# Kernel tuning notes

Measured on AMD Instinct MI355X. Metric: run time of the kernel, lower is better.

## Reference

```python
import jax, jax.numpy as jnp
import numpy as np

B, S, H = 4, 2048, 1024
NH = 16
HD = H // NH  # 64
EPS = 1e-12


def setup_inputs() -> dict:
    key = jax.random.key(0)
    ks = jax.random.split(key, 10)
    sc = 1.0 / np.sqrt(H)
    return {
        "hidden_states": jax.random.normal(ks[0], (B, S, H), jnp.float32),
        "attention_mask": jnp.ones((B, S), jnp.float32),
        "Wq": jax.random.normal(ks[1], (H, H), jnp.float32) * sc,
        "bq": jnp.zeros((H,), jnp.float32),
        "Wk": jax.random.normal(ks[2], (H, H), jnp.float32) * sc,
        "bk": jnp.zeros((H,), jnp.float32),
        "Wv": jax.random.normal(ks[3], (H, H), jnp.float32) * sc,
        "bv": jnp.zeros((H,), jnp.float32),
        "Wd": jax.random.normal(ks[4], (H, H), jnp.float32) * sc,
        "bd": jnp.zeros((H,), jnp.float32),
        "ln_g": jnp.ones((H,), jnp.float32),
        "ln_b": jnp.zeros((H,), jnp.float32),
    }


def reference(hidden_states, attention_mask, Wq, bq, Wk, bk, Wv, bv, Wd, bd, ln_g, ln_b):
    def heads(x):  # [B,S,H] -> [B,NH,S,HD]
        return x.reshape(B, S, NH, HD).transpose(0, 2, 1, 3)

    q = heads(hidden_states @ Wq.T + bq)
    k = heads(hidden_states @ Wk.T + bk)
    v = heads(hidden_states @ Wv.T + bv)

    scores = jnp.einsum('bhqd,bhkd->bhqk', q, k) / np.sqrt(HD).astype(np.float32)
    # 2D mask -> [B,1,1,S]; (1-m)*-10000 additive bias
    bias = (1.0 - attention_mask)[:, None, None, :] * -10000.0
    probs = jax.nn.softmax(scores + bias, axis=-1)  # dropout p=0 -> identity

    ctx = jnp.einsum('bhqk,bhkd->bhqd', probs, v)
    ctx = ctx.transpose(0, 2, 1, 3).reshape(B, S, H)

    out = ctx @ Wd.T + bd
    x = out + hidden_states
    mu = jnp.mean(x, axis=-1, keepdims=True)
    var = jnp.mean(jnp.square(x - mu), axis=-1, keepdims=True)
    return (x - mu) * jax.lax.rsqrt(var + EPS) * ln_g + ln_b
```

## Files before the change

kernel.cpp:

```cpp
#include <hip/hip_runtime.h>
#include <stdint.h>

#define B_ 4
#define S_ 2048
#define H_ 1024
#define NH_ 16
#define HD_ 64

typedef __bf16 bf16x8 __attribute__((ext_vector_type(8)));
typedef unsigned short u16x8 __attribute__((ext_vector_type(8)));
typedef float f32x4 __attribute__((ext_vector_type(4)));
typedef float f32x16 __attribute__((ext_vector_type(16)));

__device__ __forceinline__ unsigned short f2bf(float x) {
  union { float f; unsigned u; } c; c.f = x;
  unsigned r = (c.u + 0x7FFFu + ((c.u >> 16) & 1u)) >> 16;
  return (unsigned short)r;
}

__device__ __forceinline__ unsigned cvtpk(float lo, float hi) {
  unsigned r;
  asm("v_cvt_pk_bf16_f32 %0, %1, %2" : "=v"(r) : "v"(lo), "v"(hi));
  return r;
}

__device__ __forceinline__ void gload16(const unsigned short* g, unsigned short* lds) {
  __builtin_amdgcn_global_load_lds((const __attribute__((address_space(1))) void*)g,
                                   (__attribute__((address_space(3))) void*)lds, 16, 0, 0);
}

__global__ __launch_bounds__(256) void cvt_kernel(const float* __restrict__ src,
                                                  unsigned short* __restrict__ dst, int n) {
  int i = (blockIdx.x * blockDim.x + threadIdx.x) * 4;
  if (i < n) {
    float4 v = *reinterpret_cast<const float4*>(src + i);
    ushort4 o;
    o.x = f2bf(v.x); o.y = f2bf(v.y); o.z = f2bf(v.z); o.w = f2bf(v.w);
    *reinterpret_cast<ushort4*>(dst + i) = o;
  }
}

__global__ __launch_bounds__(256) void cvtw_kernel(const float* __restrict__ w0,
                                                   const float* __restrict__ w1,
                                                   const float* __restrict__ w2,
                                                   const float* __restrict__ w3,
                                                   unsigned short* __restrict__ o0,
                                                   unsigned short* __restrict__ o1,
                                                   unsigned short* __restrict__ o2,
                                                   unsigned short* __restrict__ o3, int n) {
  const int which = blockIdx.y;
  const float* src = (which == 0) ? w0 : (which == 1) ? w1 : (which == 2) ? w2 : w3;
  unsigned short* dst = (which == 0) ? o0 : (which == 1) ? o1 : (which == 2) ? o2 : o3;
  int i = (blockIdx.x * blockDim.x + threadIdx.x) * 4;
  if (i < n) {
    float4 v = *reinterpret_cast<const float4*>(src + i);
    ushort4 o;
    o.x = f2bf(v.x); o.y = f2bf(v.y); o.z = f2bf(v.z); o.w = f2bf(v.w);
    *reinterpret_cast<ushort4*>(dst + i) = o;
  }
}

template <bool BF16OUT>
__global__ __launch_bounds__(256) void gemm_bt(const unsigned short* __restrict__ A,
                                               const unsigned short* __restrict__ Bm,
                                               const float* __restrict__ bias,
                                               void* __restrict__ Cout,
                                               int M, int N, int K) {
  __shared__ unsigned short As[128 * 32];
  __shared__ unsigned short Bs[128 * 32];
  const int t = threadIdx.x;
  const int lane = t & 63;
  const int wv = t >> 6;
  const int wm = wv >> 1, wn = wv & 1;
  const int m0 = blockIdx.x * 128, n0 = blockIdx.y * 128;
  const int l15 = lane & 15, g8 = (lane >> 4) * 8;

  f32x4 acc[4][4];
#pragma unroll
  for (int i = 0; i < 4; ++i)
#pragma unroll
    for (int j = 0; j < 4; ++j) { f32x4 z = {0.f, 0.f, 0.f, 0.f}; acc[i][j] = z; }

  const int rowA = t >> 2;
  const int colA = (t & 3) * 8;
  const unsigned short* gA0 = A + (long)(m0 + rowA) * K + colA;
  const unsigned short* gA1 = A + (long)(m0 + 64 + rowA) * K + colA;
  const unsigned short* gB0 = Bm + (long)(n0 + rowA) * K + colA;
  const unsigned short* gB1 = Bm + (long)(n0 + 64 + rowA) * K + colA;
  unsigned short* ldsA0 = &As[wv * 512];
  unsigned short* ldsA1 = &As[2048 + wv * 512];
  unsigned short* ldsB0 = &Bs[wv * 512];
  unsigned short* ldsB1 = &Bs[2048 + wv * 512];

  for (int k0 = 0; k0 < K; k0 += 32) {
    __syncthreads();
    gload16(gA0 + k0, ldsA0);
    gload16(gA1 + k0, ldsA1);
    gload16(gB0 + k0, ldsB0);
    gload16(gB1 + k0, ldsB1);
    __syncthreads();

    bf16x8 af[4], bfr[4];
#pragma unroll
    for (int i = 0; i < 4; ++i)
      af[i] = *reinterpret_cast<const bf16x8*>(&As[(wm * 64 + i * 16 + l15) * 32 + g8]);
#pragma unroll
    for (int j = 0; j < 4; ++j)
      bfr[j] = *reinterpret_cast<const bf16x8*>(&Bs[(wn * 64 + j * 16 + l15) * 32 + g8]);
#pragma unroll
    for (int i = 0; i < 4; ++i)
#pragma unroll
      for (int j = 0; j < 4; ++j)
        acc[i][j] = __builtin_amdgcn_mfma_f32_16x16x32_bf16(af[i], bfr[j], acc[i][j], 0, 0, 0);
  }

  const int r0 = (lane >> 4) * 4;
#pragma unroll
  for (int i = 0; i < 4; ++i)
#pragma unroll
    for (int j = 0; j < 4; ++j) {
      int col = n0 + wn * 64 + j * 16 + l15;
      float bv = bias[col];
#pragma unroll
      for (int r = 0; r < 4; ++r) {
        int row = m0 + wm * 64 + i * 16 + r0 + r;
        float v = acc[i][j][r] + bv;
        if (BF16OUT)
          ((unsigned short*)Cout)[(long)row * N + col] = f2bf(v);
        else
          ((float*)Cout)[(long)row * N + col] = v;
      }
    }
}

__global__ __launch_bounds__(256) void attn_kernel(const unsigned short* __restrict__ Q,
                                                   const unsigned short* __restrict__ Kg,
                                                   const unsigned short* __restrict__ Vg,
                                                   const float* __restrict__ mask,
                                                   unsigned short* __restrict__ ctx) {
  __shared__ __align__(16) unsigned short Kt[2][64 * 64];
  __shared__ __align__(16) unsigned short VtT[2][64 * 72];
  __shared__ __align__(16) float biasL[2][64];
  __shared__ __align__(16) float alBuf[4][32];
  __shared__ int mflag[2];
  __shared__ int anyMsh;

  const int t = threadIdx.x, lane = t & 63;
  const int wv = t >> 6;
  const int id = blockIdx.x;
  const int bh = ((id >> 7) << 3) | (id & 7);
  const int qb = (id >> 3) & 15;
  const int h = bh & 15, b = bh >> 4;
  const int q0w = qb * 128 + wv * 32;
  const int l31 = lane & 31, h2 = lane >> 5;
  const long headoff = (long)h * HD_;
  const float L2E = 1.44269504088896f;
  const float SC = 0.125f * L2E;

  if (t == 0) anyMsh = 0;
  __syncthreads();
  {
    bool nz = false;
    for (int i = t; i < S_; i += 256) nz |= (mask[(long)b * S_ + i] != 1.0f);
    if (__any(nz) && lane == 0) atomicOr(&anyMsh, 1);
  }

  bf16x8 qf[4];
  {
    const unsigned short* Qrow = Q + ((long)(b * S_ + q0w + l31)) * H_ + headoff;
#pragma unroll
    for (int c = 0; c < 4; ++c) {
      bf16x8 raw = *reinterpret_cast<const bf16x8*>(Qrow + 16 * c + 8 * h2);
#pragma unroll
      for (int j = 0; j < 8; ++j) qf[c][j] = (__bf16)((float)raw[j] * SC);
    }
  }
  __syncthreads();
  const bool anyM = (anyMsh != 0);

  f32x16 o[2];
#pragma unroll
  for (int dt = 0; dt < 2; ++dt)
#pragma unroll
    for (int r = 0; r < 16; ++r) o[dt][r] = 0.f;
  float mrow = -1.0e30f, lsum = 0.f;

  int koff[4];
#pragma unroll
  for (int c = 0; c < 4; ++c) koff[c] = 8 * ((2 * c + h2) ^ (l31 & 7));

  const int rowd0 = l31, rowd1 = 32 + l31;
  const int grp0 = (rowd0 >> 3) & 7, grp1 = (rowd1 >> 3) & 7;
  int voff0[4], voff1[4];
#pragma unroll
  for (int kc = 0; kc < 4; ++kc) {
    voff0[kc] = rowd0 * 72 + 8 * ((2 * kc + h2) ^ grp0);
    voff1[kc] = rowd1 * 72 + 8 * ((2 * kc + h2) ^ grp1);
  }

  const long gbase = (long)(b * S_) * H_ + headoff;

  const unsigned short* kg0 =
      Kg + gbase + (long)(16 * wv + (lane >> 3)) * H_ + 8 * ((lane & 7) ^ (lane >> 3));
  const unsigned short* kg1 = kg0 + 8 * H_;

  const int vrow = (t >> 3) * 2, dc = t & 7;
  u16x8 vr0, vr1;

  auto LOADK = [&](int buf, int kv0) {
    gload16(kg0 + (long)kv0 * H_, &Kt[buf][(16 * wv) * 64]);
    gload16(kg1 + (long)kv0 * H_, &Kt[buf][(16 * wv + 8) * 64]);
  };
  auto LOADV = [&](int kv0) {
    vr0 = *reinterpret_cast<const u16x8*>(Vg + gbase + (long)(kv0 + vrow) * H_ + dc * 8);
    vr1 = *reinterpret_cast<const u16x8*>(Vg + gbase + (long)(kv0 + vrow + 1) * H_ + dc * 8);
  };
  auto WRITEV = [&](int buf, int kv0) {
    const int pos = (vrow & 7) | (((vrow >> 3) ^ dc) << 3);
#pragma unroll
    for (int j = 0; j < 8; ++j) {
      ushort2 pr; pr.x = vr0[j]; pr.y = vr1[j];
      *reinterpret_cast<ushort2*>(&VtT[buf][(dc * 8 + j) * 72 + pos]) = pr;
    }
    if (anyM && t < 64) {
      float mv = mask[(long)b * S_ + kv0 + t];
      biasL[buf][t] = (1.f - mv) * (-10000.f * L2E);
      unsigned long long bal = __ballot(mv != 1.0f);
      if (t == 0) mflag[buf] = (bal != 0ull);
    }
  };

  auto SMPV = [&](f32x16& sv, int kvt, int cur) {
    float m0 = fmaxf(fmaxf(sv[0], sv[1]), sv[2]);
    float m1 = fmaxf(fmaxf(sv[3], sv[4]), sv[5]);
    float m2 = fmaxf(fmaxf(sv[6], sv[7]), sv[8]);
    float m3 = fmaxf(fmaxf(sv[9], sv[10]), sv[11]);
    float m4 = fmaxf(fmaxf(sv[12], sv[13]), sv[14]);
    float t0 = fmaxf(fmaxf(m0, m1), m2);
    float t1 = fmaxf(fmaxf(m3, m4), sv[15]);
    float tm = fmaxf(t0, t1);
    tm = fmaxf(tm, __shfl_xor(tm, 32));
    if (!__all(tm <= mrow + 8.0f)) {
      float mn = fmaxf(mrow, tm);
      float al = exp2f(mrow - mn);
      mrow = mn;
      lsum *= al;
      if (lane < 32) alBuf[wv][lane] = al;
      __builtin_amdgcn_wave_barrier();
#pragma unroll
      for (int m = 0; m < 4; ++m) {
        f32x4 av = *reinterpret_cast<const f32x4*>(&alBuf[wv][8 * m + 4 * h2]);
#pragma unroll
        for (int i = 0; i < 4; ++i) {
          o[0][4 * m + i] *= av[i];
          o[1][4 * m + i] *= av[i];
        }
      }
    }
#pragma unroll
    for (int r = 0; r < 16; ++r) sv[r] = exp2f(sv[r] - mrow);
    {
      float s0 = sv[0] + sv[1], s1 = sv[2] + sv[3], s2 = sv[4] + sv[5], s3 = sv[6] + sv[7];
      float s4 = sv[8] + sv[9], s5 = sv[10] + sv[11], s6 = sv[12] + sv[13], s7 = sv[14] + sv[15];
      float u0 = s0 + s1, u1 = s2 + s3, u2 = s4 + s5, u3 = s6 + s7;
      float ts = (u0 + u1) + (u2 + u3);
      ts += __shfl_xor(ts, 32);
      lsum += ts;
    }
#pragma unroll
    for (int c2 = 0; c2 < 2; ++c2) {
      const int kc = 2 * kvt + c2;
      unsigned p0 = cvtpk(sv[8 * c2 + 0], sv[8 * c2 + 1]);
      unsigned p1 = cvtpk(sv[8 * c2 + 2], sv[8 * c2 + 3]);
      unsigned p2 = cvtpk(sv[8 * c2 + 4], sv[8 * c2 + 5]);
      unsigned p3 = cvtpk(sv[8 * c2 + 6], sv[8 * c2 + 7]);
      asm("v_permlane32_swap_b32 %0, %1" : "+v"(p0), "+v"(p2));
      asm("v_permlane32_swap_b32 %0, %1" : "+v"(p1), "+v"(p3));
      union { unsigned w[4]; bf16x8 v; } fa;
      fa.w[0] = p0; fa.w[1] = p1; fa.w[2] = p2; fa.w[3] = p3;

      bf16x8 vb0 = *reinterpret_cast<const bf16x8*>(&VtT[cur][voff0[kc]]);
      bf16x8 vb1 = *reinterpret_cast<const bf16x8*>(&VtT[cur][voff1[kc]]);
      __builtin_amdgcn_s_setprio(1);
      o[0] = __builtin_amdgcn_mfma_f32_32x32x16_bf16(fa.v, vb0, o[0], 0, 0, 0);
      o[1] = __builtin_amdgcn_mfma_f32_32x32x16_bf16(fa.v, vb1, o[1], 0, 0, 0);
      __builtin_amdgcn_s_setprio(0);
    }
  };

  const int NT = S_ / 64;
  LOADK(0, 0);
  LOADV(0);
  WRITEV(0, 0);
  __syncthreads();

  for (int it = 0; it < NT; ++it) {
    const int cur = it & 1;
    const bool more = (it + 1 < NT);
    if (more) {
      LOADK(cur ^ 1, (it + 1) * 64);
      LOADV((it + 1) * 64);
    }

#pragma unroll
    for (int kvt = 0; kvt < 2; ++kvt) {
      f32x16 sv;
#pragma unroll
      for (int r = 0; r < 16; ++r) sv[r] = 0.f;
      const int rb = (kvt * 32 + l31) * 64;
      __builtin_amdgcn_s_setprio(1);
#pragma unroll
      for (int c = 0; c < 4; ++c) {
        bf16x8 af = *reinterpret_cast<const bf16x8*>(&Kt[cur][rb + koff[c]]);
        sv = __builtin_amdgcn_mfma_f32_32x32x16_bf16(af, qf[c], sv, 0, 0, 0);
      }
      __builtin_amdgcn_s_setprio(0);
      if (anyM && mflag[cur]) {
#pragma unroll
        for (int m = 0; m < 4; ++m) {
          f32x4 bb = *reinterpret_cast<const f32x4*>(&biasL[cur][kvt * 32 + 8 * m + 4 * h2]);
#pragma unroll
          for (int i = 0; i < 4; ++i) sv[4 * m + i] += bb[i];
        }
      }
      SMPV(sv, kvt, cur);
    }

    if (more) {
      WRITEV(cur ^ 1, (it + 1) * 64);
      __syncthreads();
    }
  }

  if (lane < 32) alBuf[wv][lane] = 1.0f / lsum;
  __builtin_amdgcn_wave_barrier();
  unsigned short* ctxbase = ctx + ((long)(b * S_ + q0w + 4 * h2)) * H_ + headoff + l31;
#pragma unroll
  for (int m = 0; m < 4; ++m) {
    f32x4 iv = *reinterpret_cast<const f32x4*>(&alBuf[wv][8 * m + 4 * h2]);
#pragma unroll
    for (int i = 0; i < 4; ++i) {
#pragma unroll
      for (int dt = 0; dt < 2; ++dt)
        ctxbase[(long)(8 * m + i) * H_ + dt * 32] = f2bf(o[dt][4 * m + i] * iv[i]);
    }
  }
}

__global__ __launch_bounds__(256) void ln_kernel(const float* __restrict__ proj,
                                                 const float* __restrict__ hs,
                                                 const float* __restrict__ gam,
                                                 const float* __restrict__ bet,
                                                 float* __restrict__ out) {
  const int row = blockIdx.x;
  const int t = threadIdx.x;
  const long base = (long)row * H_ + t * 4;
  float4 a = *reinterpret_cast<const float4*>(proj + base);
  float4 hv = *reinterpret_cast<const float4*>(hs + base);
  float x0 = a.x + hv.x, x1 = a.y + hv.y, x2 = a.z + hv.z, x3 = a.w + hv.w;
  float s1 = x0 + x1 + x2 + x3;
  float s2 = x0 * x0 + x1 * x1 + x2 * x2 + x3 * x3;
#pragma unroll
  for (int off = 1; off < 64; off <<= 1) {
    s1 += __shfl_xor(s1, off);
    s2 += __shfl_xor(s2, off);
  }
  __shared__ float a1[4], a2[4];
  if ((t & 63) == 0) { a1[t >> 6] = s1; a2[t >> 6] = s2; }
  __syncthreads();
  float ts1 = a1[0] + a1[1] + a1[2] + a1[3];
  float ts2 = a2[0] + a2[1] + a2[2] + a2[3];
  float mu = ts1 * (1.0f / H_);
  float var = ts2 * (1.0f / H_) - mu * mu;
  float inv = rsqrtf(var + 1e-12f);
  float4 gv = *reinterpret_cast<const float4*>(gam + t * 4);
  float4 bb = *reinterpret_cast<const float4*>(bet + t * 4);
  float4 ov;
  ov.x = (x0 - mu) * inv * gv.x + bb.x;
  ov.y = (x1 - mu) * inv * gv.y + bb.y;
  ov.z = (x2 - mu) * inv * gv.z + bb.z;
  ov.w = (x3 - mu) * inv * gv.w + bb.w;
  *reinterpret_cast<float4*>(out + base) = ov;
}

extern "C" void kernel_launch(void* const* d_in, const int* in_sizes, int n_in,
                              void* d_out, int out_size, void* d_ws, size_t ws_size,
                              hipStream_t stream) {
  const float* hs   = (const float*)d_in[0];
  const float* mask = (const float*)d_in[1];
  const float* Wq   = (const float*)d_in[2];
  const float* bq   = (const float*)d_in[3];
  const float* Wk   = (const float*)d_in[4];
  const float* bk   = (const float*)d_in[5];
  const float* Wv   = (const float*)d_in[6];
  const float* bv   = (const float*)d_in[7];
  const float* Wd   = (const float*)d_in[8];
  const float* bd   = (const float*)d_in[9];
  const float* lng  = (const float*)d_in[10];
  const float* lnb  = (const float*)d_in[11];
  float* out = (float*)d_out;

  char* ws = (char*)d_ws;
  const size_t SZ_X = (size_t)B_ * S_ * H_ * 2;
  const size_t SZ_W = (size_t)H_ * H_ * 2;
  unsigned short* Xb  = (unsigned short*)(ws);
  unsigned short* Wqb = (unsigned short*)(ws + SZ_X);
  unsigned short* Wkb = (unsigned short*)(ws + SZ_X + SZ_W);
  unsigned short* Wvb = (unsigned short*)(ws + SZ_X + 2 * SZ_W);
  unsigned short* Wdb = (unsigned short*)(ws + SZ_X + 3 * SZ_W);
  unsigned short* Qb  = (unsigned short*)(ws + SZ_X + 4 * SZ_W);
  unsigned short* Kb  = (unsigned short*)(ws + 2 * SZ_X + 4 * SZ_W);
  unsigned short* Vb  = (unsigned short*)(ws + 3 * SZ_X + 4 * SZ_W);
  unsigned short* Cxb = (unsigned short*)(ws + 4 * SZ_X + 4 * SZ_W);
  float* Proj         = (float*)(ws + 5 * SZ_X + 4 * SZ_W);

  const int NX = B_ * S_ * H_;
  const int NW = H_ * H_;

  cvt_kernel<<<NX / 1024, 256, 0, stream>>>(hs, Xb, NX);
  dim3 gw(NW / 1024, 4);
  cvtw_kernel<<<gw, 256, 0, stream>>>(Wq, Wk, Wv, Wd, Wqb, Wkb, Wvb, Wdb, NW);

  dim3 gg(B_ * S_ / 128, H_ / 128);
  gemm_bt<true><<<gg, 256, 0, stream>>>(Xb, Wqb, bq, Qb, B_ * S_, H_, H_);
  gemm_bt<true><<<gg, 256, 0, stream>>>(Xb, Wkb, bk, Kb, B_ * S_, H_, H_);
  gemm_bt<true><<<gg, 256, 0, stream>>>(Xb, Wvb, bv, Vb, B_ * S_, H_, H_);

  attn_kernel<<<dim3((S_ / 128) * NH_ * B_), 256, 0, stream>>>(Qb, Kb, Vb, mask, Cxb);

  gemm_bt<false><<<gg, 256, 0, stream>>>(Cxb, Wdb, bd, Proj, B_ * S_, H_, H_);

  ln_kernel<<<B_ * S_, 256, 0, stream>>>(Proj, hs, lng, lnb, out);
}
```

Measured before the change: 292.8 us.

## Fuse QKV projections into one GEMM and restructure attention score loop

Concatenates the Q, K and V weights and biases into a single 3072-wide matrix so one GEMM launch produces an interleaved QKV buffer, which the attention kernel reads with a 3072 row stride. This removes two kernel launches and gives the GEMM a larger grid for better occupancy. The attention loop now issues both 32-row score MFMA groups before running softmax, and the cross-half reductions use v_permlane32_swap instead of shuffles. The cost is strided K/V/Q reads from the wider rows and higher register pressure from holding two score tiles at once.

```diff
diff --git a/kernel.cpp b/kernel.cpp
--- a/kernel.cpp
+++ b/kernel.cpp
@@ -6,6 +6,7 @@
 #define H_ 1024
 #define NH_ 16
 #define HD_ 64
+#define KS_ 3072
 
 typedef __bf16 bf16x8 __attribute__((ext_vector_type(8)));
 typedef unsigned short u16x8 __attribute__((ext_vector_type(8)));
@@ -22,6 +23,17 @@
   unsigned r;
   asm("v_cvt_pk_bf16_f32 %0, %1, %2" : "=v"(r) : "v"(lo), "v"(hi));
   return r;
+}
+
+__device__ __forceinline__ float xmax32(float x) {
+  float a = x, b = x;
+  asm("v_permlane32_swap_b32 %0, %1" : "+v"(a), "+v"(b));
+  return fmaxf(a, b);
+}
+__device__ __forceinline__ float xadd32(float x) {
+  float a = x, b = x;
+  asm("v_permlane32_swap_b32 %0, %1" : "+v"(a), "+v"(b));
+  return a + b;
 }
 
 __device__ __forceinline__ void gload16(const unsigned short* g, unsigned short* lds) {
@@ -44,19 +56,25 @@
                                                    const float* __restrict__ w1,
                                                    const float* __restrict__ w2,
                                                    const float* __restrict__ w3,
-                                                   unsigned short* __restrict__ o0,
-                                                   unsigned short* __restrict__ o1,
-                                                   unsigned short* __restrict__ o2,
-                                                   unsigned short* __restrict__ o3, int n) {
+                                                   const float* __restrict__ bq,
+                                                   const float* __restrict__ bk,
+                                                   const float* __restrict__ bv,
+                                                   unsigned short* __restrict__ wqkv,
+                                                   unsigned short* __restrict__ wd,
+                                                   float* __restrict__ bcat, int n) {
   const int which = blockIdx.y;
   const float* src = (which == 0) ? w0 : (which == 1) ? w1 : (which == 2) ? w2 : w3;
-  unsigned short* dst = (which == 0) ? o0 : (which == 1) ? o1 : (which == 2) ? o2 : o3;
+  unsigned short* dst = (which < 3) ? (wqkv + (size_t)which * n) : wd;
   int i = (blockIdx.x * blockDim.x + threadIdx.x) * 4;
   if (i < n) {
     float4 v = *reinterpret_cast<const float4*>(src + i);
     ushort4 o;
     o.x = f2bf(v.x); o.y = f2bf(v.y); o.z = f2bf(v.z); o.w = f2bf(v.w);
     *reinterpret_cast<ushort4*>(dst + i) = o;
+  }
+  if (blockIdx.x == 0 && which < 3) {
+    const float* bs = (which == 0) ? bq : (which == 1) ? bk : bv;
+    for (int j = threadIdx.x; j < H_; j += 256) bcat[which * H_ + j] = bs[j];
   }
 }
 
@@ -167,7 +185,7 @@
 
   bf16x8 qf[4];
   {
-    const unsigned short* Qrow = Q + ((long)(b * S_ + q0w + l31)) * H_ + headoff;
+    const unsigned short* Qrow = Q + ((long)(b * S_ + q0w + l31)) * KS_ + headoff;
 #pragma unroll
     for (int c = 0; c < 4; ++c) {
       bf16x8 raw = *reinterpret_cast<const bf16x8*>(Qrow + 16 * c + 8 * h2);
@@ -198,22 +216,22 @@
     voff1[kc] = rowd1 * 72 + 8 * ((2 * kc + h2) ^ grp1);
   }
 
-  const long gbase = (long)(b * S_) * H_ + headoff;
+  const long gbase = (long)(b * S_) * KS_ + headoff;
 
   const unsigned short* kg0 =
-      Kg + gbase + (long)(16 * wv + (lane >> 3)) * H_ + 8 * ((lane & 7) ^ (lane >> 3));
-  const unsigned short* kg1 = kg0 + 8 * H_;
+      Kg + gbase + (long)(16 * wv + (lane >> 3)) * KS_ + 8 * ((lane & 7) ^ (lane >> 3));
+  const unsigned short* kg1 = kg0 + 8 * KS_;
 
   const int vrow = (t >> 3) * 2, dc = t & 7;
   u16x8 vr0, vr1;
 
   auto LOADK = [&](int buf, int kv0) {
-    gload16(kg0 + (long)kv0 * H_, &Kt[buf][(16 * wv) * 64]);
-    gload16(kg1 + (long)kv0 * H_, &Kt[buf][(16 * wv + 8) * 64]);
+    gload16(kg0 + (long)kv0 * KS_, &Kt[buf][(16 * wv) * 64]);
+    gload16(kg1 + (long)kv0 * KS_, &Kt[buf][(16 * wv + 8) * 64]);
   };
   auto LOADV = [&](int kv0) {
-    vr0 = *reinterpret_cast<const u16x8*>(Vg + gbase + (long)(kv0 + vrow) * H_ + dc * 8);
-    vr1 = *reinterpret_cast<const u16x8*>(Vg + gbase + (long)(kv0 + vrow + 1) * H_ + dc * 8);
+    vr0 = *reinterpret_cast<const u16x8*>(Vg + gbase + (long)(kv0 + vrow) * KS_ + dc * 8);
+    vr1 = *reinterpret_cast<const u16x8*>(Vg + gbase + (long)(kv0 + vrow + 1) * KS_ + dc * 8);
   };
   auto WRITEV = [&](int buf, int kv0) {
     const int pos = (vrow & 7) | (((vrow >> 3) ^ dc) << 3);
@@ -238,8 +256,7 @@
     float m4 = fmaxf(fmaxf(sv[12], sv[13]), sv[14]);
     float t0 = fmaxf(fmaxf(m0, m1), m2);
     float t1 = fmaxf(fmaxf(m3, m4), sv[15]);
-    float tm = fmaxf(t0, t1);
-    tm = fmaxf(tm, __shfl_xor(tm, 32));
+    float tm = xmax32(fmaxf(t0, t1));
     if (!__all(tm <= mrow + 8.0f)) {
       float mn = fmaxf(mrow, tm);
       float al = exp2f(mrow - mn);
@@ -263,9 +280,7 @@
       float s0 = sv[0] + sv[1], s1 = sv[2] + sv[3], s2 = sv[4] + sv[5], s3 = sv[6] + sv[7];
       float s4 = sv[8] + sv[9], s5 = sv[10] + sv[11], s6 = sv[12] + sv[13], s7 = sv[14] + sv[15];
       float u0 = s0 + s1, u1 = s2 + s3, u2 = s4 + s5, u3 = s6 + s7;
-      float ts = (u0 + u1) + (u2 + u3);
-      ts += __shfl_xor(ts, 32);
-      lsum += ts;
+      lsum += xadd32((u0 + u1) + (u2 + u3));
     }
 #pragma unroll
     for (int c2 = 0; c2 < 2; ++c2) {
@@ -302,29 +317,35 @@
       LOADV((it + 1) * 64);
     }
 
-#pragma unroll
-    for (int kvt = 0; kvt < 2; ++kvt) {
-      f32x16 sv;
-#pragma unroll
-      for (int r = 0; r < 16; ++r) sv[r] = 0.f;
-      const int rb = (kvt * 32 + l31) * 64;
-      __builtin_amdgcn_s_setprio(1);
-#pragma unroll
-      for (int c = 0; c < 4; ++c) {
-        bf16x8 af = *reinterpret_cast<const bf16x8*>(&Kt[cur][rb + koff[c]]);
-        sv = __builtin_amdgcn_mfma_f32_32x32x16_bf16(af, qf[c], sv, 0, 0, 0);
+    f32x16 sv0, sv1;
+#pragma unroll
+    for (int r = 0; r < 16; ++r) { sv0[r] = 0.f; sv1[r] = 0.f; }
+    const int rb0 = l31 * 64, rb1 = (32 + l31) * 64;
+    __builtin_amdgcn_s_setprio(1);
+#pragma unroll
+    for (int c = 0; c < 4; ++c) {
+      bf16x8 af = *reinterpret_cast<const bf16x8*>(&Kt[cur][rb0 + koff[c]]);
+      sv0 = __builtin_amdgcn_mfma_f32_32x32x16_bf16(af, qf[c], sv0, 0, 0, 0);
+    }
+#pragma unroll
+    for (int c = 0; c < 4; ++c) {
+      bf16x8 af = *reinterpret_cast<const bf16x8*>(&Kt[cur][rb1 + koff[c]]);
+      sv1 = __builtin_amdgcn_mfma_f32_32x32x16_bf16(af, qf[c], sv1, 0, 0, 0);
+    }
+    __builtin_amdgcn_s_setprio(0);
+
+    if (anyM && mflag[cur]) {
+#pragma unroll
+      for (int m = 0; m < 4; ++m) {
+        f32x4 b0 = *reinterpret_cast<const f32x4*>(&biasL[cur][8 * m + 4 * h2]);
+        f32x4 b1 = *reinterpret_cast<const f32x4*>(&biasL[cur][32 + 8 * m + 4 * h2]);
+#pragma unroll
+        for (int i = 0; i < 4; ++i) { sv0[4 * m + i] += b0[i]; sv1[4 * m + i] += b1[i]; }
       }
-      __builtin_amdgcn_s_setprio(0);
-      if (anyM && mflag[cur]) {
-#pragma unroll
-        for (int m = 0; m < 4; ++m) {
-          f32x4 bb = *reinterpret_cast<const f32x4*>(&biasL[cur][kvt * 32 + 8 * m + 4 * h2]);
-#pragma unroll
-          for (int i = 0; i < 4; ++i) sv[4 * m + i] += bb[i];
-        }
-      }
-      SMPV(sv, kvt, cur);
-    }
+    }
+
+    SMPV(sv0, 0, cur);
+    SMPV(sv1, 1, cur);
 
     if (more) {
       WRITEV(cur ^ 1, (it + 1) * 64);
@@ -403,31 +424,28 @@
   char* ws = (char*)d_ws;
   const size_t SZ_X = (size_t)B_ * S_ * H_ * 2;
   const size_t SZ_W = (size_t)H_ * H_ * 2;
-  unsigned short* Xb  = (unsigned short*)(ws);
-  unsigned short* Wqb = (unsigned short*)(ws + SZ_X);
-  unsigned short* Wkb = (unsigned short*)(ws + SZ_X + SZ_W);
-  unsigned short* Wvb = (unsigned short*)(ws + SZ_X + 2 * SZ_W);
-  unsigned short* Wdb = (unsigned short*)(ws + SZ_X + 3 * SZ_W);
-  unsigned short* Qb  = (unsigned short*)(ws + SZ_X + 4 * SZ_W);
-  unsigned short* Kb  = (unsigned short*)(ws + 2 * SZ_X + 4 * SZ_W);
-  unsigned short* Vb  = (unsigned short*)(ws + 3 * SZ_X + 4 * SZ_W);
-  unsigned short* Cxb = (unsigned short*)(ws + 4 * SZ_X + 4 * SZ_W);
-  float* Proj         = (float*)(ws + 5 * SZ_X + 4 * SZ_W);
+  unsigned short* Xb    = (unsigned short*)(ws);
+  unsigned short* Wqkvb = (unsigned short*)(ws + SZ_X);
+  unsigned short* Wdb   = (unsigned short*)(ws + SZ_X + 3 * SZ_W);
+  float*          bcat  = (float*)(ws + SZ_X + 4 * SZ_W);
+  unsigned short* QKVb  = (unsigned short*)(ws + SZ_X + 4 * SZ_W + 16384);
+  unsigned short* Cxb   = (unsigned short*)(ws + 4 * SZ_X + 4 * SZ_W + 16384);
+  float*          Proj  = (float*)(ws + 5 * SZ_X + 4 * SZ_W + 16384);
 
   const int NX = B_ * S_ * H_;
   const int NW = H_ * H_;
 
   cvt_kernel<<<NX / 1024, 256, 0, stream>>>(hs, Xb, NX);
   dim3 gw(NW / 1024, 4);
-  cvtw_kernel<<<gw, 256, 0, stream>>>(Wq, Wk, Wv, Wd, Wqb, Wkb, Wvb, Wdb, NW);
+  cvtw_kernel<<<gw, 256, 0, stream>>>(Wq, Wk, Wv, Wd, bq, bk, bv, Wqkvb, Wdb, bcat, NW);
+
+  dim3 gq(B_ * S_ / 128, KS_ / 128);
+  gemm_bt<true><<<gq, 256, 0, stream>>>(Xb, Wqkvb, bcat, QKVb, B_ * S_, KS_, H_);
+
+  attn_kernel<<<dim3((S_ / 128) * NH_ * B_), 256, 0, stream>>>(
+      QKVb, QKVb + 1024, QKVb + 2048, mask, Cxb);
 
   dim3 gg(B_ * S_ / 128, H_ / 128);
-  gemm_bt<true><<<gg, 256, 0, stream>>>(Xb, Wqb, bq, Qb, B_ * S_, H_, H_);
-  gemm_bt<true><<<gg, 256, 0, stream>>>(Xb, Wkb, bk, Kb, B_ * S_, H_, H_);
-  gemm_bt<true><<<gg, 256, 0, stream>>>(Xb, Wvb, bv, Vb, B_ * S_, H_, H_);
-
-  attn_kernel<<<dim3((S_ / 128) * NH_ * B_), 256, 0, stream>>>(Qb, Kb, Vb, mask, Cxb);
-
   gemm_bt<false><<<gg, 256, 0, stream>>>(Cxb, Wdb, bd, Proj, B_ * S_, H_, H_);
 
   ln_kernel<<<B_ * S_, 256, 0, stream>>>(Proj, hs, lng, lnb, out);
```

Result: faster. 272.3 us (-7.0%).
